# Kernel tuning notes

Hardware: AMD Instinct MI355X
Metric: run time of the kernel (lower is better)

The kernel has to match this reference:

```python
import jax, jax.numpy as jnp
import numpy as np

D_MODEL = 2048
NUM_Q_HEADS = 32
NUM_KV_HEADS = 8
HEAD_DIM = D_MODEL // NUM_Q_HEADS  # 64
NUM_GROUPS = NUM_Q_HEADS // NUM_KV_HEADS  # 4
SCALE = float(np.sqrt(HEAD_DIM))


def setup_inputs() -> dict:
    key = jax.random.key(0)
    ks = jax.random.split(key, 5)
    B, S = 2, 2048
    std = 1.0 / np.sqrt(D_MODEL)
    return {
        "x": jax.random.normal(ks[0], (B, S, D_MODEL), dtype=jnp.float32),
        "W_q": jax.random.normal(ks[1], (D_MODEL, NUM_Q_HEADS * HEAD_DIM), dtype=jnp.float32) * std,
        "W_k": jax.random.normal(ks[2], (D_MODEL, NUM_KV_HEADS * HEAD_DIM), dtype=jnp.float32) * std,
        "W_v": jax.random.normal(ks[3], (D_MODEL, NUM_KV_HEADS * HEAD_DIM), dtype=jnp.float32) * std,
        "W_o": jax.random.normal(ks[4], (D_MODEL, D_MODEL), dtype=jnp.float32) * std,
    }


def reference(x, W_q, W_k, W_v, W_o):
    B, S, _ = x.shape
    # projections; weights stored as (in, out) so y = x @ W
    Q = (x @ W_q).reshape(B, S, NUM_Q_HEADS, HEAD_DIM).transpose(0, 2, 1, 3)   # [B,Hq,S,d]
    K = (x @ W_k).reshape(B, S, NUM_KV_HEADS, HEAD_DIM).transpose(0, 2, 1, 3)  # [B,Hkv,S,d]
    V = (x @ W_v).reshape(B, S, NUM_KV_HEADS, HEAD_DIM).transpose(0, 2, 1, 3)
    # repeat_interleave KV heads across groups (faithful to the original)
    K = jnp.repeat(K, NUM_GROUPS, axis=1)  # [B,Hq,S,d]
    V = jnp.repeat(V, NUM_GROUPS, axis=1)
    scores = jnp.einsum("bhqd,bhkd->bhqk", Q, K) / SCALE  # [B,Hq,S,S]
    attn = jax.nn.softmax(scores, axis=-1)
    out = jnp.einsum("bhqk,bhkd->bhqd", attn, V)  # [B,Hq,S,d]
    out = out.transpose(0, 2, 1, 3).reshape(B, S, D_MODEL)
    return out @ W_o
```

## Files before the change

kernel.cpp:

```cpp
#include <hip/hip_runtime.h>
#include <hip/hip_bf16.h>

#define D_MODEL 2048
#define NQH 32
#define NKVH 8
#define HD 64
#define SEQ 2048
#define BATCH 2
#define MTOT (BATCH * SEQ)

typedef __attribute__((ext_vector_type(8))) short short8;
typedef __attribute__((ext_vector_type(4))) float floatx4;
typedef __attribute__((ext_vector_type(16))) float f32x16;

#define QSCALE 0.18033688011112042f

#if __has_builtin(__builtin_amdgcn_exp2f)
#define EXP2(x) __builtin_amdgcn_exp2f(x)
#else
#define EXP2(x) exp2f(x)
#endif

static __device__ inline unsigned cvtpk(float lo, float hi) {
  unsigned r;
  asm("v_cvt_pk_bf16_f32 %0, %1, %2" : "=v"(r) : "v"(lo), "v"(hi));
  return r;
}
#define PLSWAP(a, b) asm("v_permlane32_swap_b32 %0, %1" : "+v"(a), "+v"(b))

__device__ inline void gload_lds16(const __hip_bfloat16* g, short* lds) {
  __builtin_amdgcn_global_load_lds(
      (const __attribute__((address_space(1))) void*)g,
      (__attribute__((address_space(3))) void*)lds, 16, 0, 0);
}

__global__ __launch_bounds__(256) void convx_k(const float* __restrict__ x,
                                               __hip_bfloat16* __restrict__ xb,
                                               int n4) {
  int i = blockIdx.x * 256 + threadIdx.x;
  int stride = gridDim.x * 256;
  for (; i < n4; i += stride) {
    float4 v = reinterpret_cast<const float4*>(x)[i];
    union { __hip_bfloat16 h[4]; uint2 u; } cv;
    cv.h[0] = __float2bfloat16(v.x);
    cv.h[1] = __float2bfloat16(v.y);
    cv.h[2] = __float2bfloat16(v.z);
    cv.h[3] = __float2bfloat16(v.w);
    reinterpret_cast<uint2*>(xb)[i] = cv.u;
  }
}

__global__ __launch_bounds__(256) void transw_all_k(
    const float* __restrict__ Wq, const float* __restrict__ Wk,
    const float* __restrict__ Wv, const float* __restrict__ Wo,
    __hip_bfloat16* __restrict__ Wqt, __hip_bfloat16* __restrict__ Wkt,
    __hip_bfloat16* __restrict__ Wvt, __hip_bfloat16* __restrict__ Wot) {
  __shared__ float t[32][33];
  const int z = blockIdx.z;
  const int Nd = (z == 1 || z == 2) ? 512 : 2048;
  const int n0 = blockIdx.x * 32;
  if (n0 >= Nd) return;
  const float* W = (z == 0) ? Wq : (z == 1) ? Wk : (z == 2) ? Wv : Wo;
  __hip_bfloat16* Wt = (z == 0) ? Wqt : (z == 1) ? Wkt : (z == 2) ? Wvt : Wot;
  const int Kd = D_MODEL;
  const int k0 = blockIdx.y * 32;
  const int tx = threadIdx.x, ty = threadIdx.y;
#pragma unroll
  for (int j = 0; j < 32; j += 8)
    t[ty + j][tx] = W[(size_t)(k0 + ty + j) * Nd + n0 + tx];
  __syncthreads();
#pragma unroll
  for (int j = 0; j < 32; j += 8)
    Wt[(size_t)(n0 + ty + j) * Kd + k0 + tx] = __float2bfloat16(t[tx][ty + j]);
}

__global__ __launch_bounds__(512, 1) void gemmqkv_k(
    const __hip_bfloat16* __restrict__ A,
    const __hip_bfloat16* __restrict__ B0,
    const __hip_bfloat16* __restrict__ B1,
    const __hip_bfloat16* __restrict__ B2,
    __hip_bfloat16* __restrict__ O0,
    __hip_bfloat16* __restrict__ O1,
    __hip_bfloat16* __restrict__ O2) {
  constexpr int Kd = D_MODEL;
  constexpr int NT = Kd / 64;

  __shared__ short Asb[2][16384];
  __shared__ short Bsb[2][12288];

  const int bid = blockIdx.x;
  const int swz = (bid & 7) * 32 + (bid >> 3);
  const int by = swz >> 4, bx = swz & 15;
  const int m0 = by * 256, n0 = bx * 192;

  const __hip_bfloat16* Ab = A + (size_t)m0 * Kd;

  const __hip_bfloat16* bp[3];
#pragma unroll
  for (int L = 0; L < 3; ++L) {
    int nr = n0 + L * 64;
    bp[L] = (nr < 2048) ? B0 + (size_t)nr * Kd
          : (nr < 2560) ? B1 + (size_t)(nr - 2048) * Kd
                        : B2 + (size_t)(nr - 2560) * Kd;
  }

  const int tid = threadIdx.x, w = tid >> 6, l = tid & 63;
  const int wm = w >> 1, wn = w & 1;
  const int lc = l & 15, l4 = l >> 4;

  const int srow = w * 8 + (l >> 3);
  const int scc = (l & 7) ^ ((l >> 3) & 7);

#define STAGE_A(L, SB, KT) \
  gload_lds16(Ab + (size_t)((L)*64 + srow) * Kd + (KT) + scc * 8, &Asb[SB][(L)*4096 + w * 512])
#define STAGE_B(L, SB, KT) \
  gload_lds16(bp[L] + (size_t)srow * Kd + (KT) + scc * 8, &Bsb[SB][(L)*4096 + w * 512])

  floatx4 acc[4][6] = {};

  int cx[2];
#pragma unroll
  for (int kk = 0; kk < 2; ++kk) cx[kk] = (((kk * 4 + l4) ^ (lc & 7)) * 8);
  const int abase = (wm * 64 + lc) * 64;
  const int bbase = (wn * 96 + lc) * 64;

  STAGE_A(0, 0, 0); STAGE_A(1, 0, 0); STAGE_A(2, 0, 0); STAGE_A(3, 0, 0);
  STAGE_B(0, 0, 0); STAGE_B(1, 0, 0); STAGE_B(2, 0, 0);
  asm volatile("s_waitcnt vmcnt(0)" ::: "memory");
  __builtin_amdgcn_s_barrier();

  short8 af[4], bfr[6];

  for (int t = 0; t < NT; ++t) {
    const int rb = t & 1, sb = rb ^ 1;
    const short* Ar = Asb[rb];
    const short* Br = Bsb[rb];

    if (t + 1 < NT) {
      const int kt = (t + 1) * 64;
      STAGE_A(0, sb, kt); STAGE_A(1, sb, kt); STAGE_A(2, sb, kt); STAGE_A(3, sb, kt);
      STAGE_B(0, sb, kt); STAGE_B(1, sb, kt); STAGE_B(2, sb, kt);
    }

#pragma unroll
    for (int kk = 0; kk < 2; ++kk) {
#pragma unroll
      for (int mi = 0; mi < 4; ++mi)
        af[mi] = *reinterpret_cast<const short8*>(&Ar[abase + mi * 1024 + cx[kk]]);
#pragma unroll
      for (int ni = 0; ni < 6; ++ni)
        bfr[ni] = *reinterpret_cast<const short8*>(&Br[bbase + ni * 1024 + cx[kk]]);
      __builtin_amdgcn_s_setprio(1);
#pragma unroll
      for (int mi = 0; mi < 4; ++mi)
#pragma unroll
        for (int ni = 0; ni < 6; ++ni)
          acc[mi][ni] = __builtin_amdgcn_mfma_f32_16x16x32_bf16(
              af[mi], bfr[ni], acc[mi][ni], 0, 0, 0);
      __builtin_amdgcn_s_setprio(0);
    }

    asm volatile("s_waitcnt vmcnt(0)" ::: "memory");
    __builtin_amdgcn_s_barrier();
  }
#undef STAGE_A
#undef STAGE_B

#pragma unroll
  for (int mi = 0; mi < 4; ++mi)
#pragma unroll
    for (int ni = 0; ni < 6; ++ni)
#pragma unroll
      for (int i = 0; i < 4; ++i) {
        int m = m0 + wm * 64 + mi * 16 + l4 * 4 + i;
        int ncol = n0 + wn * 96 + ni * 16 + lc;
        float v = acc[mi][ni][i];
        int bb = m >> 11, s = m & 2047;
        if (ncol < 2048) {
          int hh = ncol >> 6, dd = ncol & 63;
          O0[(((size_t)bb * NQH + hh) * SEQ + s) * HD + dd] = __float2bfloat16(v * QSCALE);
        } else if (ncol < 2560) {
          int c2 = ncol - 2048;
          int hh = c2 >> 6, dd = c2 & 63;
          O1[(((size_t)bb * NKVH + hh) * SEQ + s) * HD + dd] = __float2bfloat16(v);
        } else {
          int c2 = ncol - 2560;
          int hh = c2 >> 6, dd = c2 & 63;
          O2[(((size_t)bb * NKVH + hh) * HD + dd) * SEQ + s] = __float2bfloat16(v);
        }
      }
}

__global__ __launch_bounds__(512, 1) void gemmo_k(
    const __hip_bfloat16* __restrict__ A,
    const __hip_bfloat16* __restrict__ B0,
    float* __restrict__ Cf) {
  constexpr int Kd = D_MODEL;
  constexpr int NT = Kd / 64;
  constexpr int NB = 16;
  constexpr int NWG = 16 * NB;

  __shared__ short Asb[3][16384];
  __shared__ short Bsb[3][8192];

  const int bid = blockIdx.x;
  const int swz = (bid & 7) * (NWG / 8) + (bid >> 3);
  const int by = swz / NB, bx = swz % NB;
  const int m0 = by * 256, n0 = bx * 128;

  const __hip_bfloat16* Bt = B0 + (size_t)n0 * Kd;
  const __hip_bfloat16* Ab = A + (size_t)m0 * Kd;

  const int tid = threadIdx.x, w = tid >> 6, l = tid & 63;
  const int wm = w >> 1, wn = w & 1;
  const int lc = l & 15, l4 = l >> 4;

  const int srow = w * 8 + (l >> 3);
  const int scc = (l & 7) ^ ((l >> 3) & 7);

#define STAGE_A(L, SB, KT) \
  gload_lds16(Ab + (size_t)((L)*64 + srow) * Kd + (KT) + scc * 8, &Asb[SB][(L)*4096 + w * 512])
#define STAGE_B(L, SB, KT) \
  gload_lds16(Bt + (size_t)((L)*64 + srow) * Kd + (KT) + scc * 8, &Bsb[SB][(L)*4096 + w * 512])

  floatx4 acc[4][4] = {};

  int cx[2];
#pragma unroll
  for (int kk = 0; kk < 2; ++kk) cx[kk] = (((kk * 4 + l4) ^ (lc & 7)) * 8);
  const int abase = (wm * 64 + lc) * 64;
  const int bbase = (wn * 64 + lc) * 64;

  STAGE_A(0, 0, 0); STAGE_A(1, 0, 0); STAGE_A(2, 0, 0); STAGE_A(3, 0, 0);
  STAGE_B(0, 0, 0); STAGE_B(1, 0, 0);
  STAGE_A(0, 1, 64); STAGE_A(1, 1, 64); STAGE_A(2, 1, 64); STAGE_A(3, 1, 64);
  STAGE_B(0, 1, 64); STAGE_B(1, 1, 64);
  asm volatile("s_waitcnt vmcnt(6)" ::: "memory");
  __builtin_amdgcn_s_barrier();

  short8 af[4], bfr[4];

  for (int t = 0; t < NT; ++t) {
    const int rb = t % 3, sb = (t + 2) % 3;
    const int ksrc = ((t + 2) % NT) * 64;
    const short* Ar = Asb[rb];
    const short* Br = Bsb[rb];

#pragma unroll
    for (int mi = 0; mi < 4; ++mi)
      af[mi] = *reinterpret_cast<const short8*>(&Ar[abase + mi * 1024 + cx[0]]);
#pragma unroll
    for (int ni = 0; ni < 4; ++ni)
      bfr[ni] = *reinterpret_cast<const short8*>(&Br[bbase + ni * 1024 + cx[0]]);

    STAGE_A(0, sb, ksrc); STAGE_A(1, sb, ksrc); STAGE_B(0, sb, ksrc);

    __builtin_amdgcn_s_barrier();
    asm volatile("s_waitcnt lgkmcnt(0)" ::: "memory");
    __builtin_amdgcn_sched_barrier(0);
    __builtin_amdgcn_s_setprio(1);
#pragma unroll
    for (int mi = 0; mi < 4; ++mi)
#pragma unroll
      for (int ni = 0; ni < 4; ++ni)
        acc[mi][ni] = __builtin_amdgcn_mfma_f32_16x16x32_bf16(
            af[mi], bfr[ni], acc[mi][ni], 0, 0, 0);
    __builtin_amdgcn_s_setprio(0);
    __builtin_amdgcn_s_barrier();

#pragma unroll
    for (int mi = 0; mi < 4; ++mi)
      af[mi] = *reinterpret_cast<const short8*>(&Ar[abase + mi * 1024 + cx[1]]);
#pragma unroll
    for (int ni = 0; ni < 4; ++ni)
      bfr[ni] = *reinterpret_cast<const short8*>(&Br[bbase + ni * 1024 + cx[1]]);

    STAGE_A(2, sb, ksrc); STAGE_A(3, sb, ksrc); STAGE_B(1, sb, ksrc);

    asm volatile("s_waitcnt vmcnt(6)" ::: "memory");
    __builtin_amdgcn_s_barrier();
    asm volatile("s_waitcnt lgkmcnt(0)" ::: "memory");
    __builtin_amdgcn_sched_barrier(0);
    __builtin_amdgcn_s_setprio(1);
#pragma unroll
    for (int mi = 0; mi < 4; ++mi)
#pragma unroll
      for (int ni = 0; ni < 4; ++ni)
        acc[mi][ni] = __builtin_amdgcn_mfma_f32_16x16x32_bf16(
            af[mi], bfr[ni], acc[mi][ni], 0, 0, 0);
    __builtin_amdgcn_s_setprio(0);
    __builtin_amdgcn_s_barrier();
  }
#undef STAGE_A
#undef STAGE_B

#pragma unroll
  for (int mi = 0; mi < 4; ++mi)
#pragma unroll
    for (int ni = 0; ni < 4; ++ni)
#pragma unroll
      for (int i = 0; i < 4; ++i) {
        int m = m0 + wm * 64 + mi * 16 + l4 * 4 + i;
        int ncol = n0 + wn * 64 + ni * 16 + lc;
        Cf[(size_t)m * 2048 + ncol] = acc[mi][ni][i];
      }
}

__global__ __launch_bounds__(256, 4) void attn_k(const __hip_bfloat16* __restrict__ Qb,
                                                 const __hip_bfloat16* __restrict__ Kb,
                                                 const __hip_bfloat16* __restrict__ Vtb,
                                                 __hip_bfloat16* __restrict__ Ao) {
  __shared__ short Ks[2][64 * 64];
  __shared__ short Vs[2][64 * 64];
  __shared__ float Ls[4][32];

  const int bid = blockIdx.x;
  const int xcd = bid & 7, j = bid >> 3;
  const int g = xcd * 2 + (j >> 6), wv = j & 63;
  const int b = g >> 3, kh = g & 7;
  const int h = kh * 4 + (wv >> 4), qt = wv & 15;

  const int tid = threadIdx.x, w = tid >> 6, l = tid & 63;
  const int q5 = l & 31, hl = l >> 5;

  const __hip_bfloat16* Qp = Qb + (((size_t)b * NQH + h) * SEQ + qt * 128 + w * 32) * HD;
  const __hip_bfloat16* Kp = Kb + ((size_t)b * NKVH + kh) * SEQ * HD;
  const __hip_bfloat16* Vp = Vtb + ((size_t)b * NKVH + kh) * HD * SEQ;

  short8 qf[4];
#pragma unroll
  for (int ks = 0; ks < 4; ++ks)
    qf[ks] = *reinterpret_cast<const short8*>(Qp + (size_t)q5 * HD + ks * 16 + hl * 8);

  f32x16 acc0 = {}, acc1 = {};
  float lsum = 0.f;

  const int rg = l >> 3, lc8 = l & 7;
  const int cc0 = lc8 ^ ((2 * w) & 7);
  const int cc1 = lc8 ^ ((2 * w + 1) & 7);
  const __hip_bfloat16* sK0 = Kp + (size_t)(16 * w + rg) * HD + cc0 * 8;
  const __hip_bfloat16* sK1 = Kp + (size_t)(16 * w + 8 + rg) * HD + cc1 * 8;
  const __hip_bfloat16* sV0 = Vp + (size_t)(16 * w + rg) * SEQ + cc0 * 8;
  const __hip_bfloat16* sV1 = Vp + (size_t)(16 * w + 8 + rg) * SEQ + cc1 * 8;

  int fo[4], fo1[4];
  const int ky0 = (q5 >> 3) & 7;
  const int ky1 = ((q5 + 32) >> 3) & 7;
#pragma unroll
  for (int jj = 0; jj < 4; ++jj) {
    fo[jj] = q5 * 64 + (((jj * 2 + hl) ^ ky0) * 8);
    fo1[jj] = (q5 + 32) * 64 + (((jj * 2 + hl) ^ ky1) * 8);
  }

  gload_lds16(sK0, &Ks[0][1024 * w]);
  gload_lds16(sK1, &Ks[0][1024 * w + 512]);
  gload_lds16(sV0, &Vs[0][1024 * w]);
  gload_lds16(sV1, &Vs[0][1024 * w + 512]);
  sK0 += 64 * HD; sK1 += 64 * HD; sV0 += 64; sV1 += 64;
  __syncthreads();

  for (int kb = 0; kb < SEQ / 64; ++kb) {
    const short* Kt = Ks[kb & 1];
    const short* Vt = Vs[kb & 1];

    if (kb + 1 < SEQ / 64) {
      short* Kn = Ks[(kb & 1) ^ 1];
      short* Vn = Vs[(kb & 1) ^ 1];
      gload_lds16(sK0, &Kn[1024 * w]);
      gload_lds16(sK1, &Kn[1024 * w + 512]);
      gload_lds16(sV0, &Vn[1024 * w]);
      gload_lds16(sV1, &Vn[1024 * w + 512]);
      sK0 += 64 * HD; sK1 += 64 * HD; sV0 += 64; sV1 += 64;
    }

    short8 kf0[4], kf1[4];
#pragma unroll
    for (int ks = 0; ks < 4; ++ks) {
      kf0[ks] = *reinterpret_cast<const short8*>(&Kt[fo[ks]]);
      kf1[ks] = *reinterpret_cast<const short8*>(&Kt[fo1[ks]]);
    }
    f32x16 st0 = {}, st1 = {};
    __builtin_amdgcn_s_setprio(1);
#pragma unroll
    for (int ks = 0; ks < 4; ++ks) {
      st0 = __builtin_amdgcn_mfma_f32_32x32x16_bf16(kf0[ks], qf[ks], st0, 0, 0, 0);
      st1 = __builtin_amdgcn_mfma_f32_32x32x16_bf16(kf1[ks], qf[ks], st1, 0, 0, 0);
    }
    __builtin_amdgcn_s_setprio(0);

    float ps = 0.f;
    unsigned u0[8], u1[8];
#pragma unroll
    for (int jj = 0; jj < 8; ++jj) {
      float e0 = EXP2(st0[2 * jj]), e1 = EXP2(st0[2 * jj + 1]);
      float f0 = EXP2(st1[2 * jj]), f1 = EXP2(st1[2 * jj + 1]);
      ps += (e0 + e1) + (f0 + f1);
      u0[jj] = cvtpk(e0, e1);
      u1[jj] = cvtpk(f0, f1);
    }
    lsum += ps;

    short8 vf0[4], vf1[4];
#pragma unroll
    for (int t = 0; t < 4; ++t) {
      vf0[t] = *reinterpret_cast<const short8*>(&Vt[fo[t]]);
      vf1[t] = *reinterpret_cast<const short8*>(&Vt[fo1[t]]);
    }

    PLSWAP(u0[0], u0[2]); PLSWAP(u0[1], u0[3]);
    PLSWAP(u0[4], u0[6]); PLSWAP(u0[5], u0[7]);
    PLSWAP(u1[0], u1[2]); PLSWAP(u1[1], u1[3]);
    PLSWAP(u1[4], u1[6]); PLSWAP(u1[5], u1[7]);

    __builtin_amdgcn_s_setprio(1);
#pragma unroll
    for (int t = 0; t < 4; ++t) {
      union { unsigned w4[4]; short8 s8; } pa;
      pa.w4[0] = (t >> 1 ? u1 : u0)[(t & 1) * 4 + 0];
      pa.w4[1] = (t >> 1 ? u1 : u0)[(t & 1) * 4 + 1];
      pa.w4[2] = (t >> 1 ? u1 : u0)[(t & 1) * 4 + 2];
      pa.w4[3] = (t >> 1 ? u1 : u0)[(t & 1) * 4 + 3];
      acc0 = __builtin_amdgcn_mfma_f32_32x32x16_bf16(pa.s8, vf0[t], acc0, 0, 0, 0);
      acc1 = __builtin_amdgcn_mfma_f32_32x32x16_bf16(pa.s8, vf1[t], acc1, 0, 0, 0);
    }
    __builtin_amdgcn_s_setprio(0);
    __syncthreads();
  }

  {
    float v = lsum;
    v += __shfl_xor(v, 32);
    if (l < 32) Ls[w][l] = v;
  }
  __syncthreads();

  const size_t obase = (size_t)b * SEQ + qt * 128 + w * 32;
  float inv[16];
#pragma unroll
  for (int r = 0; r < 16; ++r)
    inv[r] = 1.0f / Ls[w][(r & 3) + 8 * (r >> 2) + 4 * hl];
#pragma unroll
  for (int r = 0; r < 16; ++r) {
    int q = (r & 3) + 8 * (r >> 2) + 4 * hl;
    Ao[(obase + q) * D_MODEL + h * HD + q5] = __float2bfloat16(acc0[r] * inv[r]);
    Ao[(obase + q) * D_MODEL + h * HD + 32 + q5] = __float2bfloat16(acc1[r] * inv[r]);
  }
}

extern "C" void kernel_launch(void* const* d_in, const int* in_sizes, int n_in,
                              void* d_out, int out_size, void* d_ws, size_t ws_size,
                              hipStream_t stream) {
  const float* x  = (const float*)d_in[0];
  const float* Wq = (const float*)d_in[1];
  const float* Wk = (const float*)d_in[2];
  const float* Wv = (const float*)d_in[3];
  const float* Wo = (const float*)d_in[4];
  float* out = (float*)d_out;

  __hip_bfloat16* p = (__hip_bfloat16*)d_ws;
  __hip_bfloat16* xb  = p;
  __hip_bfloat16* Wqt = xb  + (size_t)MTOT * D_MODEL;
  __hip_bfloat16* Wkt = Wqt + (size_t)D_MODEL * D_MODEL;
  __hip_bfloat16* Wvt = Wkt + (size_t)512 * D_MODEL;
  __hip_bfloat16* Wot = Wvt + (size_t)512 * D_MODEL;
  __hip_bfloat16* Qb  = Wot + (size_t)D_MODEL * D_MODEL;
  __hip_bfloat16* Kb  = Qb  + (size_t)MTOT * D_MODEL;
  __hip_bfloat16* Vtb = Kb  + (size_t)BATCH * NKVH * SEQ * HD;
  __hip_bfloat16* Ab  = Vtb + (size_t)BATCH * NKVH * SEQ * HD;

  convx_k<<<2048, 256, 0, stream>>>(x, xb, MTOT * D_MODEL / 4);
  transw_all_k<<<dim3(64, 64, 4), dim3(32, 8), 0, stream>>>(Wq, Wk, Wv, Wo,
                                                            Wqt, Wkt, Wvt, Wot);

  gemmqkv_k<<<dim3(256), 512, 0, stream>>>(xb, Wqt, Wkt, Wvt, Qb, Kb, Vtb);
  attn_k<<<dim3(1024), 256, 0, stream>>>(Qb, Kb, Vtb, Ab);
  gemmo_k<<<dim3(256), 512, 0, stream>>>(Ab, Wot, out);
}
```

Baseline: 223.9 us.

## Merge prep kernels, triple-buffer B in QKV GEMM, simplify attention LDS swizzle

Folds the x-to-bf16 conversion into the weight transpose kernel as an extra grid slice, removing one launch. The QKV GEMM gets a third B buffer so weight tiles are prefetched two steps ahead, with partial vmcnt waits instead of full drains. The attention kernel switches to a row-based XOR swizzle so one set of fragment offsets (plus a constant) replaces two, reducing address registers. The extra LDS buffer raises shared memory use, and the waitcnt counts must match the number of outstanding loads.

```diff
diff --git a/kernel.cpp b/kernel.cpp
--- a/kernel.cpp
+++ b/kernel.cpp
@@ -34,29 +34,32 @@
       (__attribute__((address_space(3))) void*)lds, 16, 0, 0);
 }
 
-__global__ __launch_bounds__(256) void convx_k(const float* __restrict__ x,
-                                               __hip_bfloat16* __restrict__ xb,
-                                               int n4) {
-  int i = blockIdx.x * 256 + threadIdx.x;
-  int stride = gridDim.x * 256;
-  for (; i < n4; i += stride) {
-    float4 v = reinterpret_cast<const float4*>(x)[i];
-    union { __hip_bfloat16 h[4]; uint2 u; } cv;
-    cv.h[0] = __float2bfloat16(v.x);
-    cv.h[1] = __float2bfloat16(v.y);
-    cv.h[2] = __float2bfloat16(v.z);
-    cv.h[3] = __float2bfloat16(v.w);
-    reinterpret_cast<uint2*>(xb)[i] = cv.u;
-  }
-}
-
-__global__ __launch_bounds__(256) void transw_all_k(
+__global__ __launch_bounds__(256) void prep_k(
     const float* __restrict__ Wq, const float* __restrict__ Wk,
     const float* __restrict__ Wv, const float* __restrict__ Wo,
     __hip_bfloat16* __restrict__ Wqt, __hip_bfloat16* __restrict__ Wkt,
-    __hip_bfloat16* __restrict__ Wvt, __hip_bfloat16* __restrict__ Wot) {
+    __hip_bfloat16* __restrict__ Wvt, __hip_bfloat16* __restrict__ Wot,
+    const float* __restrict__ x, __hip_bfloat16* __restrict__ xb) {
   __shared__ float t[32][33];
   const int z = blockIdx.z;
+  const int tx = threadIdx.x, ty = threadIdx.y;
+
+  if (z == 4) {
+    int flat = (blockIdx.y * 64 + blockIdx.x) * 256 + ty * 32 + tx;
+#pragma unroll
+    for (int rep = 0; rep < 2; ++rep) {
+      int i = flat + rep * (64 * 64 * 256);
+      float4 v = reinterpret_cast<const float4*>(x)[i];
+      union { __hip_bfloat16 h[4]; uint2 u; } cv;
+      cv.h[0] = __float2bfloat16(v.x);
+      cv.h[1] = __float2bfloat16(v.y);
+      cv.h[2] = __float2bfloat16(v.z);
+      cv.h[3] = __float2bfloat16(v.w);
+      reinterpret_cast<uint2*>(xb)[i] = cv.u;
+    }
+    return;
+  }
+
   const int Nd = (z == 1 || z == 2) ? 512 : 2048;
   const int n0 = blockIdx.x * 32;
   if (n0 >= Nd) return;
@@ -64,7 +67,6 @@
   __hip_bfloat16* Wt = (z == 0) ? Wqt : (z == 1) ? Wkt : (z == 2) ? Wvt : Wot;
   const int Kd = D_MODEL;
   const int k0 = blockIdx.y * 32;
-  const int tx = threadIdx.x, ty = threadIdx.y;
 #pragma unroll
   for (int j = 0; j < 32; j += 8)
     t[ty + j][tx] = W[(size_t)(k0 + ty + j) * Nd + n0 + tx];
@@ -86,7 +88,7 @@
   constexpr int NT = Kd / 64;
 
   __shared__ short Asb[2][16384];
-  __shared__ short Bsb[2][12288];
+  __shared__ short Bsb[3][12288];
 
   const int bid = blockIdx.x;
   const int swz = (bid & 7) * 32 + (bid >> 3);
@@ -126,19 +128,22 @@
 
   STAGE_A(0, 0, 0); STAGE_A(1, 0, 0); STAGE_A(2, 0, 0); STAGE_A(3, 0, 0);
   STAGE_B(0, 0, 0); STAGE_B(1, 0, 0); STAGE_B(2, 0, 0);
-  asm volatile("s_waitcnt vmcnt(0)" ::: "memory");
+  STAGE_B(0, 1, 64); STAGE_B(1, 1, 64); STAGE_B(2, 1, 64);
+  asm volatile("s_waitcnt vmcnt(3)" ::: "memory");
   __builtin_amdgcn_s_barrier();
 
   short8 af[4], bfr[6];
 
   for (int t = 0; t < NT; ++t) {
-    const int rb = t & 1, sb = rb ^ 1;
-    const short* Ar = Asb[rb];
-    const short* Br = Bsb[rb];
+    const short* Ar = Asb[t & 1];
+    const short* Br = Bsb[t % 3];
 
     if (t + 1 < NT) {
-      const int kt = (t + 1) * 64;
-      STAGE_A(0, sb, kt); STAGE_A(1, sb, kt); STAGE_A(2, sb, kt); STAGE_A(3, sb, kt);
+      const int kt = (t + 1) * 64, sa = (t + 1) & 1;
+      STAGE_A(0, sa, kt); STAGE_A(1, sa, kt); STAGE_A(2, sa, kt); STAGE_A(3, sa, kt);
+    }
+    if (t + 2 < NT) {
+      const int kt = (t + 2) * 64, sb = (t + 2) % 3;
       STAGE_B(0, sb, kt); STAGE_B(1, sb, kt); STAGE_B(2, sb, kt);
     }
 
@@ -160,7 +165,10 @@
       __builtin_amdgcn_s_setprio(0);
     }
 
-    asm volatile("s_waitcnt vmcnt(0)" ::: "memory");
+    if (t < NT - 2)
+      asm volatile("s_waitcnt vmcnt(3)" ::: "memory");
+    else
+      asm volatile("s_waitcnt vmcnt(0)" ::: "memory");
     __builtin_amdgcn_s_barrier();
   }
 #undef STAGE_A
@@ -335,28 +343,22 @@
   f32x16 acc0 = {}, acc1 = {};
   float lsum = 0.f;
 
-  const int rg = l >> 3, lc8 = l & 7;
-  const int cc0 = lc8 ^ ((2 * w) & 7);
-  const int cc1 = lc8 ^ ((2 * w + 1) & 7);
-  const __hip_bfloat16* sK0 = Kp + (size_t)(16 * w + rg) * HD + cc0 * 8;
-  const __hip_bfloat16* sK1 = Kp + (size_t)(16 * w + 8 + rg) * HD + cc1 * 8;
-  const __hip_bfloat16* sV0 = Vp + (size_t)(16 * w + rg) * SEQ + cc0 * 8;
-  const __hip_bfloat16* sV1 = Vp + (size_t)(16 * w + 8 + rg) * SEQ + cc1 * 8;
-
-  int fo[4], fo1[4];
-  const int ky0 = (q5 >> 3) & 7;
-  const int ky1 = ((q5 + 32) >> 3) & 7;
-#pragma unroll
-  for (int jj = 0; jj < 4; ++jj) {
-    fo[jj] = q5 * 64 + (((jj * 2 + hl) ^ ky0) * 8);
-    fo1[jj] = (q5 + 32) * 64 + (((jj * 2 + hl) ^ ky1) * 8);
-  }
-
-  gload_lds16(sK0, &Ks[0][1024 * w]);
-  gload_lds16(sK1, &Ks[0][1024 * w + 512]);
-  gload_lds16(sV0, &Vs[0][1024 * w]);
-  gload_lds16(sV1, &Vs[0][1024 * w + 512]);
-  sK0 += 64 * HD; sK1 += 64 * HD; sV0 += 64; sV1 += 64;
+  const int rg = l >> 3;
+  const int cc = (l & 7) ^ (rg & 7);
+  const __hip_bfloat16* sK = Kp + (size_t)(16 * w + rg) * HD + cc * 8;
+  const __hip_bfloat16* sV = Vp + (size_t)(16 * w + rg) * SEQ + cc * 8;
+
+  int fo[4];
+#pragma unroll
+  for (int jj = 0; jj < 4; ++jj)
+    fo[jj] = q5 * 64 + (((jj * 2 + hl) ^ (q5 & 7)) * 8);
+
+  gload_lds16(sK, &Ks[0][1024 * w]);
+  gload_lds16(sK + 8 * HD, &Ks[0][1024 * w + 512]);
+  gload_lds16(sV, &Vs[0][1024 * w]);
+  gload_lds16(sV + 8 * (size_t)SEQ, &Vs[0][1024 * w + 512]);
+  sK += 64 * HD;
+  sV += 64;
   __syncthreads();
 
   for (int kb = 0; kb < SEQ / 64; ++kb) {
@@ -366,18 +368,19 @@
     if (kb + 1 < SEQ / 64) {
       short* Kn = Ks[(kb & 1) ^ 1];
       short* Vn = Vs[(kb & 1) ^ 1];
-      gload_lds16(sK0, &Kn[1024 * w]);
-      gload_lds16(sK1, &Kn[1024 * w + 512]);
-      gload_lds16(sV0, &Vn[1024 * w]);
-      gload_lds16(sV1, &Vn[1024 * w + 512]);
-      sK0 += 64 * HD; sK1 += 64 * HD; sV0 += 64; sV1 += 64;
+      gload_lds16(sK, &Kn[1024 * w]);
+      gload_lds16(sK + 8 * HD, &Kn[1024 * w + 512]);
+      gload_lds16(sV, &Vn[1024 * w]);
+      gload_lds16(sV + 8 * (size_t)SEQ, &Vn[1024 * w + 512]);
+      sK += 64 * HD;
+      sV += 64;
     }
 
     short8 kf0[4], kf1[4];
 #pragma unroll
     for (int ks = 0; ks < 4; ++ks) {
       kf0[ks] = *reinterpret_cast<const short8*>(&Kt[fo[ks]]);
-      kf1[ks] = *reinterpret_cast<const short8*>(&Kt[fo1[ks]]);
+      kf1[ks] = *reinterpret_cast<const short8*>(&Kt[fo[ks] + 2048]);
     }
     f32x16 st0 = {}, st1 = {};
     __builtin_amdgcn_s_setprio(1);
@@ -404,7 +407,7 @@
 #pragma unroll
     for (int t = 0; t < 4; ++t) {
       vf0[t] = *reinterpret_cast<const short8*>(&Vt[fo[t]]);
-      vf1[t] = *reinterpret_cast<const short8*>(&Vt[fo1[t]]);
+      vf1[t] = *reinterpret_cast<const short8*>(&Vt[fo[t] + 2048]);
     }
 
     PLSWAP(u0[0], u0[2]); PLSWAP(u0[1], u0[3]);
@@ -468,9 +471,8 @@
   __hip_bfloat16* Vtb = Kb  + (size_t)BATCH * NKVH * SEQ * HD;
   __hip_bfloat16* Ab  = Vtb + (size_t)BATCH * NKVH * SEQ * HD;
 
-  convx_k<<<2048, 256, 0, stream>>>(x, xb, MTOT * D_MODEL / 4);
-  transw_all_k<<<dim3(64, 64, 4), dim3(32, 8), 0, stream>>>(Wq, Wk, Wv, Wo,
-                                                            Wqt, Wkt, Wvt, Wot);
+  prep_k<<<dim3(64, 64, 5), dim3(32, 8), 0, stream>>>(Wq, Wk, Wv, Wo,
+                                                      Wqt, Wkt, Wvt, Wot, x, xb);
 
   gemmqkv_k<<<dim3(256), 512, 0, stream>>>(xb, Wqt, Wkt, Wvt, Qb, Kb, Vtb);
   attn_k<<<dim3(1024), 256, 0, stream>>>(Qb, Kb, Vtb, Ab);
```

Result: faster. 216.7 us (-3.2%).
